# Kernel optimization log

Measured on AMD Instinct MI355X. Metric: run time of the kernel, lower is better.

Reference implementation:

```python
import jax, jax.numpy as jnp
import numpy as np

N = 65536   # total nodes
E = 1048576 # total edges (avg degree 16)
B = 512     # graphs in batch
H = 4       # gat1 heads
C = 64      # per-head channels / GNN_HIDDEN


def segment_softmax(logits, seg, num_segments):
    # numerically stable softmax over segments (PyG softmax semantics, eps=1e-16)
    m = jax.ops.segment_max(logits, seg, num_segments=num_segments)
    m = jnp.where(jnp.isfinite(m), m, 0.0)
    e = jnp.exp(logits - m[seg])
    s = jax.ops.segment_sum(e, seg, num_segments=num_segments)
    return e / (s[seg] + 1e-16)


def gat_conv(x, edge_index, edge_attr, W, att_src, att_dst, We, att_edge, bias, heads, out_ch, concat):
    # PyG GATConv with edge_dim, add_self_loops=False
    n = x.shape[0]
    h = (x @ W).reshape(n, heads, out_ch)                 # (N,H,C)
    src, dst = edge_index[0], edge_index[1]
    a_s = jnp.sum(h * att_src, axis=-1)                   # (N,H)
    a_d = jnp.sum(h * att_dst, axis=-1)                   # (N,H)
    he = (edge_attr @ We).reshape(-1, heads, out_ch)      # (E,H,C)
    a_e = jnp.sum(he * att_edge, axis=-1)                 # (E,H)
    alpha = jax.nn.leaky_relu(a_s[src] + a_d[dst] + a_e, negative_slope=0.2)
    alpha = segment_softmax(alpha, dst, n)                # softmax over incoming edges per dst
    out = jax.ops.segment_sum(h[src] * alpha[..., None], dst, num_segments=n)  # (N,H,C)
    out = out.reshape(n, heads * out_ch) if concat else out.mean(axis=1)
    return out + bias


def setup_inputs() -> dict:
    key = jax.random.key(0)
    ks = jax.random.split(key, 24)
    s = 0.05
    d = {}
    d["global_feat"] = jax.random.normal(ks[0], (B, 512), jnp.float32)
    d["x"] = jax.random.normal(ks[1], (N, 13), jnp.float32)
    d["roi_feats"] = jax.random.normal(ks[2], (N, 256), jnp.float32)
    d["edge_index"] = jax.random.randint(ks[3], (2, E), 0, N)
    d["edge_attr"] = jax.random.normal(ks[4], (E, 5), jnp.float32)
    d["batch_vec"] = jnp.sort(jax.random.randint(ks[5], (N,), 0, B))
    # roi_proj / scene_proj
    d["roi_W"] = jax.random.normal(ks[6], (256, 64), jnp.float32) * s
    d["roi_b"] = jnp.zeros((64,), jnp.float32)
    d["scene_W"] = jax.random.normal(ks[7], (512, 128), jnp.float32) * s
    d["scene_b"] = jnp.zeros((128,), jnp.float32)
    d["g1_W"] = jax.random.normal(ks[8], (77, H * C), jnp.float32) * s
    d["g1_att_src"] = jax.random.normal(ks[9], (H, C), jnp.float32) * s
    d["g1_att_dst"] = jax.random.normal(ks[10], (H, C), jnp.float32) * s
    d["g1_We"] = jax.random.normal(ks[11], (5, H * C), jnp.float32) * s
    d["g1_att_edge"] = jax.random.normal(ks[12], (H, C), jnp.float32) * s
    d["g1_bias"] = jnp.zeros((H * C,), jnp.float32)
    # gat2: 256 -> 64, 1 head
    d["g2_W"] = jax.random.normal(ks[13], (H * C, C), jnp.float32) * s
    d["g2_att_src"] = jax.random.normal(ks[14], (1, C), jnp.float32) * s
    d["g2_att_dst"] = jax.random.normal(ks[15], (1, C), jnp.float32) * s
    d["g2_We"] = jax.random.normal(ks[16], (5, C), jnp.float32) * s
    d["g2_att_edge"] = jax.random.normal(ks[17], (1, C), jnp.float32) * s
    d["g2_bias"] = jnp.zeros((C,), jnp.float32)
    # attention pooling gate + classifier
    d["gate_W"] = jax.random.normal(ks[18], (C, 1), jnp.float32) * s
    d["gate_b"] = jnp.zeros((1,), jnp.float32)
    d["cls1_W"] = jax.random.normal(ks[19], (128 + C, 64), jnp.float32) * s
    d["cls1_b"] = jnp.zeros((64,), jnp.float32)
    d["cls2_W"] = jax.random.normal(ks[20], (64, 3), jnp.float32) * s
    d["cls2_b"] = jnp.zeros((3,), jnp.float32)
    return d


def reference(global_feat, x, roi_feats, edge_index, edge_attr, batch_vec,
              roi_W, roi_b, scene_W, scene_b,
              g1_W, g1_att_src, g1_att_dst, g1_We, g1_att_edge, g1_bias,
              g2_W, g2_att_src, g2_att_dst, g2_We, g2_att_edge, g2_bias,
              gate_W, gate_b, cls1_W, cls1_b, cls2_W, cls2_b):
    scene = global_feat @ scene_W + scene_b                       # (B,128)
    vis = jax.nn.relu(roi_feats @ roi_W + roi_b)                  # (N,64)
    h = jnp.concatenate([x, vis], axis=-1)                        # (N,77)
    h = jax.nn.relu(gat_conv(h, edge_index, edge_attr, g1_W, g1_att_src, g1_att_dst, g1_We, g1_att_edge, g1_bias, H, C, True))
    h = gat_conv(h, edge_index, edge_attr, g2_W, g2_att_src, g2_att_dst, g2_We, g2_att_edge, g2_bias, 1, C, False)  # (N,64)
    # GlobalAttention pooling
    gate = segment_softmax((h @ gate_W + gate_b)[:, 0], batch_vec, B)
    rel = jax.ops.segment_sum(gate[:, None] * h, batch_vec, num_segments=B)  # (B,64)
    comb = jnp.concatenate([scene, rel], axis=-1)                 # (B,192)
    hid = jax.nn.relu(comb @ cls1_W + cls1_b)                     # dropout off (eval)
    return hid @ cls2_W + cls2_b                                  # (B,3)
```

## Files before the change

kernel.cpp:

```cpp
#include <hip/hip_runtime.h>

#define N_NODES 65536
#define N_EDGES 1048576
#define NB      512

typedef unsigned short u16;
typedef unsigned int   u32;
typedef unsigned long long u64;

__device__ __forceinline__ float bf2f(u16 u) { return __uint_as_float(((u32)u) << 16); }
__device__ __forceinline__ float lo16(u32 u) { return __uint_as_float(u << 16); }
__device__ __forceinline__ float hi16(u32 u) { return __uint_as_float(u & 0xffff0000u); }
__device__ __forceinline__ u16 f2bf(float f) {
    u32 u = __float_as_uint(f);
    u32 r = (u + 0x7fffu + ((u >> 16) & 1u)) >> 16;
    return (u16)r;
}
__device__ __forceinline__ float wsum(float v) {
    for (int o = 32; o; o >>= 1) v += __shfl_xor(v, o, 64);
    return v;
}
__device__ __forceinline__ float wmax(float v) {
    for (int o = 32; o; o >>= 1) v = fmaxf(v, __shfl_xor(v, o, 64));
    return v;
}

__global__ void k_prep(const float* g1We, const float* g1ae, const float* g2We, const float* g2ae,
                       float* M1, float* M2) {
    int t = threadIdx.x;
    if (t < 20) {
        int j = t >> 2, h = t & 3;
        float s = 0.f;
        for (int c = 0; c < 64; c++) s += g1We[j * 256 + h * 64 + c] * g1ae[h * 64 + c];
        M1[t] = s;
    } else if (t < 25) {
        int j = t - 20;
        float s = 0.f;
        for (int c = 0; c < 64; c++) s += g2We[j * 64 + c] * g2ae[c];
        M2[j] = s;
    }
}

__global__ __launch_bounds__(256) void k_scene(const float* __restrict__ gf, const float* __restrict__ W,
                                               const float* __restrict__ bias, float* __restrict__ scene) {
    int idx = blockIdx.x * 256 + threadIdx.x;
    int b = idx >> 7, j = idx & 127;
    float acc = 0.f;
    for (int k = 0; k < 512; k++) acc += gf[b * 512 + k] * W[k * 128 + j];
    scene[idx] = acc + bias[j];
}

__global__ __launch_bounds__(256) void k_hist(const int* ei, int* cnt) {
    int e = blockIdx.x * 256 + threadIdx.x;
    atomicAdd(&cnt[ei[N_EDGES + e]], 1);
}

__global__ __launch_bounds__(256) void k_scan_blk(const int* __restrict__ cnt, int* __restrict__ pre,
                                                  int* __restrict__ bsum) {
    __shared__ int sd[256];
    int t = threadIdx.x, b = blockIdx.x;
    int base = b * 1024 + t * 4;
    int4 c = *(const int4*)(cnt + base);
    int s = c.x + c.y + c.z + c.w;
    sd[t] = s;
    __syncthreads();
    for (int off = 1; off < 256; off <<= 1) {
        int v = (t >= off) ? sd[t - off] : 0;
        __syncthreads();
        sd[t] += v;
        __syncthreads();
    }
    int excl = sd[t] - s;
    int4 p;
    p.x = excl;
    p.y = excl + c.x;
    p.z = excl + c.x + c.y;
    p.w = excl + c.x + c.y + c.z;
    *(int4*)(pre + base) = p;
    if (t == 255) bsum[b] = sd[255];
}

__global__ __launch_bounds__(64) void k_scan_top(int* bsum) {
    int t = threadIdx.x;
    int v = bsum[t];
    int inc = v;
    for (int off = 1; off < 64; off <<= 1) {
        int u = __shfl_up(inc, off, 64);
        if (t >= off) inc += u;
    }
    bsum[t] = inc - v;
}

__global__ __launch_bounds__(256) void k_scan_fix(const int* __restrict__ pre, const int* __restrict__ bsum,
                                                  int* __restrict__ row_ptr, int* __restrict__ coarse_cur) {
    int i = blockIdx.x * 256 + threadIdx.x;
    int v = pre[i] + bsum[i >> 10];
    row_ptr[i] = v;
    if ((i & 255) == 0) coarse_cur[i >> 8] = v;
    if (i == 0) row_ptr[N_NODES] = N_EDGES;
}

__global__ __launch_bounds__(256) void k_bucket(const int* __restrict__ ei, int* coarse_cur,
                                                u32* __restrict__ bpack, int* __restrict__ bsrc) {
    __shared__ u32 stageP[4096];
    __shared__ int stageS[4096];
    __shared__ int bcnt[256], bscan[256], boff[256], gbase[256];
    int t = threadIdx.x;
    int e0 = blockIdx.x * 4096;
    bcnt[t] = 0;
    __syncthreads();
    int dreg[16], sreg[16];
    for (int it = 0; it < 16; it++) {
        int e = e0 + it * 256 + t;
        int dd = ei[N_EDGES + e];
        dreg[it] = dd;
        sreg[it] = ei[e];
        atomicAdd(&bcnt[dd >> 8], 1);
    }
    __syncthreads();
    int v = bcnt[t];
    bscan[t] = v;
    __syncthreads();
    for (int off = 1; off < 256; off <<= 1) {
        int u = (t >= off) ? bscan[t - off] : 0;
        __syncthreads();
        bscan[t] += u;
        __syncthreads();
    }
    boff[t] = bscan[t] - v;
    gbase[t] = v ? atomicAdd(&coarse_cur[t], v) : 0;
    __syncthreads();
    for (int it = 0; it < 16; it++) {
        int e = e0 + it * 256 + t;
        int b = dreg[it] >> 8;
        int pos = atomicAdd(&boff[b], 1);
        stageP[pos] = ((u32)e << 12) | (u32)(dreg[it] & 255);
        stageS[pos] = sreg[it];
    }
    __syncthreads();
    for (int idx = t; idx < 4096; idx += 256) {
        int lo = 0, hi = 255;
        while (lo < hi) { int mid = (lo + hi) >> 1; if (bscan[mid] > idx) hi = mid; else lo = mid + 1; }
        int b = lo;
        int g = gbase[b] + (idx - (bscan[b] - bcnt[b]));
        bpack[g] = stageP[idx];
        bsrc[g] = stageS[idx];
    }
}

__global__ __launch_bounds__(256) void k_sortb(const u32* __restrict__ bpack, const int* __restrict__ bsrc,
                                               const int* __restrict__ row_ptr,
                                               int* __restrict__ eord, int* __restrict__ ssrc) {
    __shared__ int cur[256];
    int t = threadIdx.x, b = blockIdx.x;
    int nbase = b * 256;
    cur[t] = row_ptr[nbase + t];
    __syncthreads();
    int beg = row_ptr[nbase];
    int end = row_ptr[nbase + 256];
    for (int i = beg + t; i < end; i += 256) {
        u32 wd = bpack[i];
        int src = bsrc[i];
        int d8 = wd & 255;
        int pos = atomicAdd(&cur[d8], 1);
        eord[pos] = (int)(wd >> 12);
        ssrc[pos] = src;
    }
}

__global__ __launch_bounds__(256) void k_payload(const int* __restrict__ eord, const float* __restrict__ ea,
                                                 const float* __restrict__ M1, const float* __restrict__ M2,
                                                 float* __restrict__ a1es, float* __restrict__ a2es) {
    int pos = blockIdx.x * 256 + threadIdx.x;
    int e = eord[pos];
    float v[5];
    for (int j = 0; j < 5; j++) v[j] = ea[(size_t)e * 5 + j];
    float4 o;
    o.x = v[0]*M1[0]  + v[1]*M1[4]  + v[2]*M1[8]  + v[3]*M1[12] + v[4]*M1[16];
    o.y = v[0]*M1[1]  + v[1]*M1[5]  + v[2]*M1[9]  + v[3]*M1[13] + v[4]*M1[17];
    o.z = v[0]*M1[2]  + v[1]*M1[6]  + v[2]*M1[10] + v[3]*M1[14] + v[4]*M1[18];
    o.w = v[0]*M1[3]  + v[1]*M1[7]  + v[2]*M1[11] + v[3]*M1[15] + v[4]*M1[19];
    *(float4*)(a1es + (size_t)pos * 4) = o;
    a2es[pos] = v[0]*M2[0] + v[1]*M2[1] + v[2]*M2[2] + v[3]*M2[3] + v[4]*M2[4];
}

__global__ __launch_bounds__(256) void k_vis(const float* __restrict__ A, const float* __restrict__ W,
                                             const float* __restrict__ bias, float* __restrict__ out) {
    __shared__ float At[64][68];
    __shared__ float Wl[64][68];
    int t = threadIdx.x;
    int n0 = blockIdx.x * 64;
    int cg = t & 15, rg = t >> 4;
    int sr = t >> 2, scs = (t & 3) * 16;
    float acc[4][4];
    for (int i = 0; i < 4; i++) for (int j = 0; j < 4; j++) acc[i][j] = 0.f;
    for (int kc = 0; kc < 4; kc++) {
        __syncthreads();
        const float* ap = A + (size_t)(n0 + sr) * 256 + kc * 64 + scs;
        float4 q0 = *(const float4*)ap, q1 = *(const float4*)(ap + 4);
        float4 q2 = *(const float4*)(ap + 8), q3 = *(const float4*)(ap + 12);
        At[scs + 0][sr] = q0.x;  At[scs + 1][sr] = q0.y;  At[scs + 2][sr] = q0.z;  At[scs + 3][sr] = q0.w;
        At[scs + 4][sr] = q1.x;  At[scs + 5][sr] = q1.y;  At[scs + 6][sr] = q1.z;  At[scs + 7][sr] = q1.w;
        At[scs + 8][sr] = q2.x;  At[scs + 9][sr] = q2.y;  At[scs + 10][sr] = q2.z; At[scs + 11][sr] = q2.w;
        At[scs + 12][sr] = q3.x; At[scs + 13][sr] = q3.y; At[scs + 14][sr] = q3.z; At[scs + 15][sr] = q3.w;
        const float* wp = W + (size_t)(kc * 64 + sr) * 64 + scs;
        *(float4*)&Wl[sr][scs + 0]  = *(const float4*)wp;
        *(float4*)&Wl[sr][scs + 4]  = *(const float4*)(wp + 4);
        *(float4*)&Wl[sr][scs + 8]  = *(const float4*)(wp + 8);
        *(float4*)&Wl[sr][scs + 12] = *(const float4*)(wp + 12);
        __syncthreads();
        for (int k = 0; k < 64; k++) {
            float4 a4 = *(const float4*)&At[k][rg * 4];
            float4 w4 = *(const float4*)&Wl[k][cg * 4];
            acc[0][0] += a4.x * w4.x; acc[0][1] += a4.x * w4.y; acc[0][2] += a4.x * w4.z; acc[0][3] += a4.x * w4.w;
            acc[1][0] += a4.y * w4.x; acc[1][1] += a4.y * w4.y; acc[1][2] += a4.y * w4.z; acc[1][3] += a4.y * w4.w;
            acc[2][0] += a4.z * w4.x; acc[2][1] += a4.z * w4.y; acc[2][2] += a4.z * w4.z; acc[2][3] += a4.z * w4.w;
            acc[3][0] += a4.w * w4.x; acc[3][1] += a4.w * w4.y; acc[3][2] += a4.w * w4.z; acc[3][3] += a4.w * w4.w;
        }
    }
    float4 bb = *(const float4*)(bias + cg * 4);
    for (int i = 0; i < 4; i++) {
        float4 o;
        o.x = fmaxf(acc[i][0] + bb.x, 0.f);
        o.y = fmaxf(acc[i][1] + bb.y, 0.f);
        o.z = fmaxf(acc[i][2] + bb.z, 0.f);
        o.w = fmaxf(acc[i][3] + bb.w, 0.f);
        *(float4*)(out + (size_t)(n0 + rg * 4 + i) * 64 + cg * 4) = o;
    }
}

__global__ __launch_bounds__(256) void k_h2(const u16* __restrict__ A, const float* __restrict__ W,
                                            u16* __restrict__ out) {
    __shared__ float At[64][68];
    __shared__ float Wl[64][68];
    int t = threadIdx.x;
    int n0 = blockIdx.x * 64;
    int cg = t & 15, rg = t >> 4;
    int sr = t >> 2, scs = (t & 3) * 16;
    float acc[4][4];
    for (int i = 0; i < 4; i++) for (int j = 0; j < 4; j++) acc[i][j] = 0.f;
    for (int kc = 0; kc < 4; kc++) {
        __syncthreads();
        const u16* ap = A + (size_t)(n0 + sr) * 256 + kc * 64 + scs;
        uint4 u0 = *(const uint4*)ap;
        uint4 u1 = *(const uint4*)(ap + 8);
        At[scs + 0][sr] = lo16(u0.x);  At[scs + 1][sr] = hi16(u0.x);
        At[scs + 2][sr] = lo16(u0.y);  At[scs + 3][sr] = hi16(u0.y);
        At[scs + 4][sr] = lo16(u0.z);  At[scs + 5][sr] = hi16(u0.z);
        At[scs + 6][sr] = lo16(u0.w);  At[scs + 7][sr] = hi16(u0.w);
        At[scs + 8][sr] = lo16(u1.x);  At[scs + 9][sr] = hi16(u1.x);
        At[scs + 10][sr] = lo16(u1.y); At[scs + 11][sr] = hi16(u1.y);
        At[scs + 12][sr] = lo16(u1.z); At[scs + 13][sr] = hi16(u1.z);
        At[scs + 14][sr] = lo16(u1.w); At[scs + 15][sr] = hi16(u1.w);
        const float* wp = W + (size_t)(kc * 64 + sr) * 64 + scs;
        *(float4*)&Wl[sr][scs + 0]  = *(const float4*)wp;
        *(float4*)&Wl[sr][scs + 4]  = *(const float4*)(wp + 4);
        *(float4*)&Wl[sr][scs + 8]  = *(const float4*)(wp + 8);
        *(float4*)&Wl[sr][scs + 12] = *(const float4*)(wp + 12);
        __syncthreads();
        for (int k = 0; k < 64; k++) {
            float4 a4 = *(const float4*)&At[k][rg * 4];
            float4 w4 = *(const float4*)&Wl[k][cg * 4];
            acc[0][0] += a4.x * w4.x; acc[0][1] += a4.x * w4.y; acc[0][2] += a4.x * w4.z; acc[0][3] += a4.x * w4.w;
            acc[1][0] += a4.y * w4.x; acc[1][1] += a4.y * w4.y; acc[1][2] += a4.y * w4.z; acc[1][3] += a4.y * w4.w;
            acc[2][0] += a4.z * w4.x; acc[2][1] += a4.z * w4.y; acc[2][2] += a4.z * w4.z; acc[2][3] += a4.z * w4.w;
            acc[3][0] += a4.w * w4.x; acc[3][1] += a4.w * w4.y; acc[3][2] += a4.w * w4.z; acc[3][3] += a4.w * w4.w;
        }
    }
    u32* outu = (u32*)out;
    for (int i = 0; i < 4; i++) {
        uint2 pk;
        pk.x = (u32)f2bf(acc[i][0]) | ((u32)f2bf(acc[i][1]) << 16);
        pk.y = (u32)f2bf(acc[i][2]) | ((u32)f2bf(acc[i][3]) << 16);
        *(uint2*)(outu + (size_t)(n0 + rg * 4 + i) * 32 + cg * 2) = pk;
    }
}

__global__ __launch_bounds__(256) void k_h1(const float* __restrict__ x, const float* __restrict__ vis,
                                            const float* __restrict__ g1W, u16* __restrict__ h1) {
    __shared__ float At[77][36];
    __shared__ float Wl[77][132];
    int t = threadIdx.x, ch = blockIdx.y;
    int n0 = blockIdx.x * 32;
    int cg = t & 31, rg = t >> 5;
    for (int idx = t; idx < 9856; idx += 256) {
        int k = idx >> 7, c = idx & 127;
        Wl[k][c] = g1W[(size_t)k * 256 + ch * 128 + c];
    }
    for (int idx = t; idx < 2464; idx += 256) {
        int r = idx / 77, k = idx - r * 77;
        At[k][r] = (k < 13) ? x[(size_t)(n0 + r) * 13 + k] : vis[(size_t)(n0 + r) * 64 + (k - 13)];
    }
    __syncthreads();
    float acc[4][4];
    for (int i = 0; i < 4; i++) for (int j = 0; j < 4; j++) acc[i][j] = 0.f;
    for (int k = 0; k < 77; k++) {
        float4 a4 = *(const float4*)&At[k][rg * 4];
        float4 w4 = *(const float4*)&Wl[k][cg * 4];
        acc[0][0] += a4.x * w4.x; acc[0][1] += a4.x * w4.y; acc[0][2] += a4.x * w4.z; acc[0][3] += a4.x * w4.w;
        acc[1][0] += a4.y * w4.x; acc[1][1] += a4.y * w4.y; acc[1][2] += a4.y * w4.z; acc[1][3] += a4.y * w4.w;
        acc[2][0] += a4.z * w4.x; acc[2][1] += a4.z * w4.y; acc[2][2] += a4.z * w4.z; acc[2][3] += a4.z * w4.w;
        acc[3][0] += a4.w * w4.x; acc[3][1] += a4.w * w4.y; acc[3][2] += a4.w * w4.z; acc[3][3] += a4.w * w4.w;
    }
    for (int i = 0; i < 4; i++) {
        uint2 pk;
        pk.x = (u32)f2bf(acc[i][0]) | ((u32)f2bf(acc[i][1]) << 16);
        pk.y = (u32)f2bf(acc[i][2]) | ((u32)f2bf(acc[i][3]) << 16);
        *(uint2*)(h1 + (size_t)(n0 + rg * 4 + i) * 256 + ch * 128 + cg * 4) = pk;
    }
}

__global__ __launch_bounds__(256) void k_a1(const u16* __restrict__ h1, const float* __restrict__ as_,
                                            const float* __restrict__ ad_, float* a1s, float* a1d) {
    int t = threadIdx.x;
    int w = t >> 6, L = t & 63;
    float4 as4 = *(const float4*)(as_ + 4 * L);
    float4 ad4 = *(const float4*)(ad_ + 4 * L);
    int base = (blockIdx.x * 4 + w) * 16;
    for (int j = 0; j < 16; j++) {
        int n = base + j;
        uint2 u = *((const uint2*)(h1 + (size_t)n * 256) + L);
        float v0 = lo16(u.x), v1 = hi16(u.x), v2 = lo16(u.y), v3 = hi16(u.y);
        float ps = v0 * as4.x + v1 * as4.y + v2 * as4.z + v3 * as4.w;
        float pd = v0 * ad4.x + v1 * ad4.y + v2 * ad4.z + v3 * ad4.w;
        for (int o = 1; o < 16; o <<= 1) { ps += __shfl_xor(ps, o, 64); pd += __shfl_xor(pd, o, 64); }
        if ((L & 15) == 0) {
            a1s[n * 4 + (L >> 4)] = ps;
            a1d[n * 4 + (L >> 4)] = pd;
        }
    }
}

__global__ __launch_bounds__(256) void k_a2(const u16* __restrict__ h2b, const float* __restrict__ as_,
                                            const float* __restrict__ ad_, float* a2s, float* a2d) {
    int t = threadIdx.x;
    int w = t >> 6, lane = t & 63;
    int n = blockIdx.x * 4 + w;
    float v = bf2f(h2b[(size_t)n * 64 + lane]);
    float ps = wsum(v * as_[lane]);
    float pd = wsum(v * ad_[lane]);
    if (lane == 0) { a2s[n] = ps; a2d[n] = pd; }
}

__global__ __launch_bounds__(256) void k_soft1(const int* __restrict__ row_ptr, const int* __restrict__ ssrc,
                                               const float* __restrict__ a1s, const float* __restrict__ a1d,
                                               const float* __restrict__ a1es, float* __restrict__ w1) {
    int t = threadIdx.x;
    int wv = t >> 6, L = t & 63;
    int n = blockIdx.x * 4 + wv;
    int h = L >> 4, j = L & 15;
    int beg = row_ptr[n], deg = row_ptr[n + 1] - beg;
    if (deg == 0) return;
    float adn = a1d[n * 4 + h];
    float m = -3.0e38f, s = 0.f;
    for (int i = j; i < deg; i += 16) {
        int pos = beg + i;
        float l = a1s[ssrc[pos] * 4 + h] + adn + a1es[(size_t)pos * 4 + h];
        l = (l > 0.f) ? l : 0.2f * l;
        if (l > m) { s = s * __expf(m - l) + 1.f; m = l; }
        else       { s += __expf(l - m); }
    }
    for (int o = 1; o < 16; o <<= 1) {
        float mo = __shfl_xor(m, o, 64), so = __shfl_xor(s, o, 64);
        float M = fmaxf(m, mo);
        s = s * __expf(m - M) + so * __expf(mo - M);
        m = M;
    }
    float inv = 1.f / (s + 1e-16f);
    for (int i = j; i < deg; i += 16) {
        int pos = beg + i;
        float l = a1s[ssrc[pos] * 4 + h] + adn + a1es[(size_t)pos * 4 + h];
        l = (l > 0.f) ? l : 0.2f * l;
        w1[(size_t)pos * 4 + h] = __expf(l - m) * inv;
    }
}

__global__ __launch_bounds__(256) void k_gath1(const int* __restrict__ row_ptr, const int* __restrict__ ssrc,
                                               const float* __restrict__ w1, const u16* __restrict__ h1,
                                               const float* __restrict__ bias, u16* __restrict__ out1) {
    int t = threadIdx.x;
    int wv = t >> 6, L = t & 63;
    int n = blockIdx.x * 4 + wv;
    int beg = row_ptr[n], deg = row_ptr[n + 1] - beg;
    int hd = L >> 4, j16 = L & 15;
    float a0 = 0.f, a1v = 0.f, a2v = 0.f, a3v = 0.f;
    int base = 0;
    for (; base + 16 <= deg; base += 16) {
        int idx = beg + base + j16;
        int src_r = ssrc[idx];
        float w_r = w1[(size_t)idx * 4 + hd];
        #pragma unroll
        for (int j = 0; j < 16; j++) {
            int src = __shfl(src_r, j, 64);
            float wgt = __shfl(w_r, hd * 16 + j, 64);
            uint2 ua = *((const uint2*)(h1 + (size_t)src * 256) + L);
            a0  += wgt * lo16(ua.x);
            a1v += wgt * hi16(ua.x);
            a2v += wgt * lo16(ua.y);
            a3v += wgt * hi16(ua.y);
        }
    }
    int cnt = deg - base;
    if (cnt > 0) {
        int idx = beg + base + j16;
        int src_r = 0; float w_r = 0.f;
        if (j16 < cnt) {
            src_r = ssrc[idx];
            w_r = w1[(size_t)idx * 4 + hd];
        }
        for (int j = 0; j < cnt; j++) {
            int src = __shfl(src_r, j, 64);
            float wgt = __shfl(w_r, hd * 16 + j, 64);
            uint2 ua = *((const uint2*)(h1 + (size_t)src * 256) + L);
            a0  += wgt * lo16(ua.x);
            a1v += wgt * hi16(ua.x);
            a2v += wgt * lo16(ua.y);
            a3v += wgt * hi16(ua.y);
        }
    }
    float4 bb = *(const float4*)(bias + 4 * L);
    uint2 pk;
    pk.x = (u32)f2bf(fmaxf(a0 + bb.x, 0.f)) | ((u32)f2bf(fmaxf(a1v + bb.y, 0.f)) << 16);
    pk.y = (u32)f2bf(fmaxf(a2v + bb.z, 0.f)) | ((u32)f2bf(fmaxf(a3v + bb.w, 0.f)) << 16);
    *((uint2*)(out1 + (size_t)n * 256) + L) = pk;
}

__global__ __launch_bounds__(256) void k_soft2(const int* __restrict__ row_ptr, const int* __restrict__ ssrc,
                                               const float* __restrict__ a2s, const float* __restrict__ a2d,
                                               const float* __restrict__ a2es, float* __restrict__ w2) {
    int t = threadIdx.x;
    int wv = t >> 6, L = t & 63;
    int g = L >> 4, j = L & 15;
    int n = blockIdx.x * 16 + wv * 4 + g;
    int beg = row_ptr[n], deg = row_ptr[n + 1] - beg;
    if (deg == 0) return;
    float adn = a2d[n];
    float m = -3.0e38f, s = 0.f;
    for (int i = j; i < deg; i += 16) {
        int pos = beg + i;
        float l = a2s[ssrc[pos]] + adn + a2es[pos];
        l = (l > 0.f) ? l : 0.2f * l;
        if (l > m) { s = s * __expf(m - l) + 1.f; m = l; }
        else       { s += __expf(l - m); }
    }
    for (int o = 1; o < 16; o <<= 1) {
        float mo = __shfl_xor(m, o, 64), so = __shfl_xor(s, o, 64);
        float M = fmaxf(m, mo);
        s = s * __expf(m - M) + so * __expf(mo - M);
        m = M;
    }
    float inv = 1.f / (s + 1e-16f);
    for (int i = j; i < deg; i += 16) {
        int pos = beg + i;
        float l = a2s[ssrc[pos]] + adn + a2es[pos];
        l = (l > 0.f) ? l : 0.2f * l;
        w2[pos] = __expf(l - m) * inv;
    }
}

__global__ __launch_bounds__(256) void k_gath2(const int* __restrict__ row_ptr, const int* __restrict__ ssrc,
                                               const float* __restrict__ w2, const u16* __restrict__ h2b,
                                               const float* __restrict__ bias, float* __restrict__ hfin) {
    int t = threadIdx.x;
    int wv = t >> 6, L = t & 63;
    int n = blockIdx.x * 4 + wv;
    int beg = row_ptr[n], deg = row_ptr[n + 1] - beg;
    float acc = 0.f;
    for (int base = 0; base < deg; base += 64) {
        int cnt = min(64, deg - base);
        int src_r = 0; float w_r = 0.f;
        if (L < cnt) {
            src_r = ssrc[beg + base + L];
            w_r = w2[beg + base + L];
        }
        int j = 0;
        for (; j + 4 <= cnt; j += 4) {
            int s0 = __shfl(src_r, j, 64),     s1 = __shfl(src_r, j + 1, 64);
            int s2 = __shfl(src_r, j + 2, 64), s3 = __shfl(src_r, j + 3, 64);
            float w0 = __shfl(w_r, j, 64),     w1v = __shfl(w_r, j + 1, 64);
            float w2v = __shfl(w_r, j + 2, 64), w3 = __shfl(w_r, j + 3, 64);
            float v0 = bf2f(h2b[(size_t)s0 * 64 + L]);
            float v1 = bf2f(h2b[(size_t)s1 * 64 + L]);
            float v2 = bf2f(h2b[(size_t)s2 * 64 + L]);
            float v3 = bf2f(h2b[(size_t)s3 * 64 + L]);
            acc += w0 * v0 + w1v * v1 + w2v * v2 + w3 * v3;
        }
        for (; j < cnt; j++) {
            int s0 = __shfl(src_r, j, 64);
            float w0 = __shfl(w_r, j, 64);
            acc += w0 * bf2f(h2b[(size_t)s0 * 64 + L]);
        }
    }
    hfin[(size_t)n * 64 + L] = acc + bias[L];
}

__global__ __launch_bounds__(64) void k_pool(const int* __restrict__ bvec, const float* __restrict__ hf,
                                             const float* gateW, const float* gateb,
                                             const float* __restrict__ scene,
                                             const float* c1W, const float* c1b,
                                             const float* c2W, const float* c2b,
                                             float* __restrict__ outp) {
    int b = blockIdx.x, lane = threadIdx.x;
    __shared__ float gwl[64], se[64], comb[192], hid[64];
    gwl[lane] = gateW[lane];
    __syncthreads();
    int s0, s1;
    { int lo = 0, hi = N_NODES; while (lo < hi) { int mid = (lo + hi) >> 1; if (bvec[mid] < b) lo = mid + 1; else hi = mid; } s0 = lo; }
    { int lo = 0, hi = N_NODES; while (lo < hi) { int mid = (lo + hi) >> 1; if (bvec[mid] < b + 1) lo = mid + 1; else hi = mid; } s1 = lo; }
    float gb = gateb[0];
    float m = -3.0e38f, ssum = 0.f, acc = 0.f;
    for (int cs = s0; cs < s1; cs += 64) {
        int cnt = min(64, s1 - cs);
        float l = -3.0e38f;
        if (lane < cnt) {
            int n = cs + lane;
            float d = 0.f;
            for (int i = 0; i < 64; i++) d += hf[(size_t)n * 64 + i] * gwl[i];
            l = d + gb;
        }
        float cm = wmax(l);
        float newm = fmaxf(m, cm);
        float rsc = __expf(m - newm);
        float e = (lane < cnt) ? __expf(l - newm) : 0.f;
        float es = wsum(e);
        ssum = ssum * rsc + es;
        se[lane] = e;
        __syncthreads();
        float a2 = 0.f;
        for (int i = 0; i < cnt; i++) a2 += se[i] * hf[(size_t)(cs + i) * 64 + lane];
        acc = acc * rsc + a2;
        __syncthreads();
        m = newm;
    }
    float rel = acc / (ssum + 1e-16f);
    comb[lane] = scene[b * 128 + lane];
    comb[64 + lane] = scene[b * 128 + 64 + lane];
    comb[128 + lane] = rel;
    __syncthreads();
    float hj = 0.f;
    for (int k = 0; k < 192; k++) hj += comb[k] * c1W[k * 64 + lane];
    hj += c1b[lane];
    hid[lane] = fmaxf(hj, 0.f);
    __syncthreads();
    if (lane < 3) {
        float o = 0.f;
        for (int k = 0; k < 64; k++) o += hid[k] * c2W[k * 3 + lane];
        o += c2b[lane];
        outp[b * 3 + lane] = o;
    }
}

extern "C" void kernel_launch(void* const* d_in, const int* in_sizes, int n_in,
                              void* d_out, int out_size, void* d_ws, size_t ws_size,
                              hipStream_t stream) {
    (void)in_sizes; (void)n_in; (void)out_size; (void)ws_size;
    const float* gf     = (const float*)d_in[0];
    const float* x      = (const float*)d_in[1];
    const float* roi    = (const float*)d_in[2];
    const int*   ei     = (const int*)d_in[3];
    const float* ea     = (const float*)d_in[4];
    const int*   bvec   = (const int*)d_in[5];
    const float* roiW   = (const float*)d_in[6];
    const float* roib   = (const float*)d_in[7];
    const float* sceneW = (const float*)d_in[8];
    const float* sceneb = (const float*)d_in[9];
    const float* g1W    = (const float*)d_in[10];
    const float* g1as   = (const float*)d_in[11];
    const float* g1ad   = (const float*)d_in[12];
    const float* g1We   = (const float*)d_in[13];
    const float* g1ae   = (const float*)d_in[14];
    const float* g1b    = (const float*)d_in[15];
    const float* g2W    = (const float*)d_in[16];
    const float* g2as   = (const float*)d_in[17];
    const float* g2ad   = (const float*)d_in[18];
    const float* g2We   = (const float*)d_in[19];
    const float* g2ae   = (const float*)d_in[20];
    const float* g2b    = (const float*)d_in[21];
    const float* gateW  = (const float*)d_in[22];
    const float* gateb  = (const float*)d_in[23];
    const float* c1W    = (const float*)d_in[24];
    const float* c1b    = (const float*)d_in[25];
    const float* c2W    = (const float*)d_in[26];
    const float* c2b    = (const float*)d_in[27];

    char* w = (char*)d_ws;
    size_t o = 0;
    auto nxt = [&](size_t bytes) -> char* {
        char* p = w + o;
        o += (bytes + 255) & ~(size_t)255;
        return p;
    };
    float* scene  = (float*)nxt((size_t)NB * 128 * 4);
    float* M1     = (float*)nxt(80);
    float* M2     = (float*)nxt(32);
    int* cnt      = (int*)nxt((size_t)N_NODES * 4);
    int* pre      = (int*)nxt((size_t)N_NODES * 4);
    int* bsum     = (int*)nxt(64 * 4);
    int* row_ptr  = (int*)nxt((size_t)(N_NODES + 1) * 4);
    int* coarse   = (int*)nxt(256 * 4);
    u32* bpack    = (u32*)nxt((size_t)N_EDGES * 4);
    int* bsrc     = (int*)nxt((size_t)N_EDGES * 4);
    int* eord     = (int*)nxt((size_t)N_EDGES * 4);
    int* ssrc     = (int*)nxt((size_t)N_EDGES * 4);
    float* a1es   = (float*)nxt((size_t)N_EDGES * 16);
    float* a2es   = (float*)nxt((size_t)N_EDGES * 4);
    float* visbuf = (float*)nxt((size_t)N_NODES * 64 * 4);
    u16* h1       = (u16*)nxt((size_t)N_NODES * 256 * 2);
    u16* out1     = (u16*)nxt((size_t)N_NODES * 256 * 2);
    float* w1buf  = (float*)nxt((size_t)N_EDGES * 16);
    float* hfin   = (float*)nxt((size_t)N_NODES * 64 * 4);
    float* a1s    = (float*)nxt((size_t)N_NODES * 16);
    float* a1d    = (float*)nxt((size_t)N_NODES * 16);
    float* a2s    = (float*)nxt((size_t)N_NODES * 4);
    float* a2d    = (float*)nxt((size_t)N_NODES * 4);

    float* vis = visbuf;
    float* w2  = visbuf;
    float* w1  = w1buf;
    u16*   h2b = (u16*)w1buf;

    hipMemsetAsync(cnt, 0, (size_t)N_NODES * 4, stream);
    k_prep<<<1, 32, 0, stream>>>(g1We, g1ae, g2We, g2ae, M1, M2);
    k_scene<<<(NB * 128) / 256, 256, 0, stream>>>(gf, sceneW, sceneb, scene);
    k_hist<<<N_EDGES / 256, 256, 0, stream>>>(ei, cnt);
    k_scan_blk<<<64, 256, 0, stream>>>(cnt, pre, bsum);
    k_scan_top<<<1, 64, 0, stream>>>(bsum);
    k_scan_fix<<<N_NODES / 256, 256, 0, stream>>>(pre, bsum, row_ptr, coarse);
    k_bucket<<<256, 256, 0, stream>>>(ei, coarse, bpack, bsrc);
    k_sortb<<<256, 256, 0, stream>>>(bpack, bsrc, row_ptr, eord, ssrc);
    k_payload<<<N_EDGES / 256, 256, 0, stream>>>(eord, ea, M1, M2, a1es, a2es);
    k_vis<<<N_NODES / 64, 256, 0, stream>>>(roi, roiW, roib, vis);
    k_h1<<<dim3(N_NODES / 32, 2), 256, 0, stream>>>(x, vis, g1W, h1);
    k_a1<<<N_NODES / 64, 256, 0, stream>>>(h1, g1as, g1ad, a1s, a1d);
    k_soft1<<<N_NODES / 4, 256, 0, stream>>>(row_ptr, ssrc, a1s, a1d, a1es, w1);
    k_gath1<<<N_NODES / 4, 256, 0, stream>>>(row_ptr, ssrc, w1, h1, g1b, out1);
    k_h2<<<N_NODES / 64, 256, 0, stream>>>(out1, g2W, h2b);
    k_a2<<<N_NODES / 4, 256, 0, stream>>>(h2b, g2as, g2ad, a2s, a2d);
    k_soft2<<<N_NODES / 16, 256, 0, stream>>>(row_ptr, ssrc, a2s, a2d, a2es, w2);
    k_gath2<<<N_NODES / 4, 256, 0, stream>>>(row_ptr, ssrc, w2, h2b, g2b, hfin);
    k_pool<<<NB, 64, 0, stream>>>(bvec, hfin, gateW, gateb, scene, c1W, c1b, c2W, c2b, (float*)d_out);
}
```

Before: 657.8 us.

## Split wavefront into two edge-halves with wider row loads in GAT gathers

Both gather kernels now split each 64-lane wavefront into two 32-lane halves that process different edges at once. Each lane loads wider vectors: 16 bytes per lane for the 4-head layer and 4 bytes for the 64-channel layer. Each half handles two edges per iteration, and the halves' partial sums are combined with a cross-half shuffle before the bias and store. The intent is more memory-level parallelism and fewer, wider random row loads per edge, replacing the shuffle-broadcast of indices with direct per-lane index loads. Costs include redundant index and weight loads across lanes, more accumulator registers, and a final reduction step.

Result: faster. 640.9 us (-2.6%).

```diff
diff --git a/kernel.cpp b/kernel.cpp
--- a/kernel.cpp
+++ b/kernel.cpp
@@ -382,47 +382,44 @@
     int wv = t >> 6, L = t & 63;
     int n = blockIdx.x * 4 + wv;
     int beg = row_ptr[n], deg = row_ptr[n + 1] - beg;
-    int hd = L >> 4, j16 = L & 15;
-    float a0 = 0.f, a1v = 0.f, a2v = 0.f, a3v = 0.f;
-    int base = 0;
-    for (; base + 16 <= deg; base += 16) {
-        int idx = beg + base + j16;
-        int src_r = ssrc[idx];
-        float w_r = w1[(size_t)idx * 4 + hd];
-        #pragma unroll
-        for (int j = 0; j < 16; j++) {
-            int src = __shfl(src_r, j, 64);
-            float wgt = __shfl(w_r, hd * 16 + j, 64);
-            uint2 ua = *((const uint2*)(h1 + (size_t)src * 256) + L);
-            a0  += wgt * lo16(ua.x);
-            a1v += wgt * hi16(ua.x);
-            a2v += wgt * lo16(ua.y);
-            a3v += wgt * hi16(ua.y);
-        }
-    }
-    int cnt = deg - base;
-    if (cnt > 0) {
-        int idx = beg + base + j16;
-        int src_r = 0; float w_r = 0.f;
-        if (j16 < cnt) {
-            src_r = ssrc[idx];
-            w_r = w1[(size_t)idx * 4 + hd];
-        }
-        for (int j = 0; j < cnt; j++) {
-            int src = __shfl(src_r, j, 64);
-            float wgt = __shfl(w_r, hd * 16 + j, 64);
-            uint2 ua = *((const uint2*)(h1 + (size_t)src * 256) + L);
-            a0  += wgt * lo16(ua.x);
-            a1v += wgt * hi16(ua.x);
-            a2v += wgt * lo16(ua.y);
-            a3v += wgt * hi16(ua.y);
-        }
-    }
-    float4 bb = *(const float4*)(bias + 4 * L);
-    uint2 pk;
-    pk.x = (u32)f2bf(fmaxf(a0 + bb.x, 0.f)) | ((u32)f2bf(fmaxf(a1v + bb.y, 0.f)) << 16);
-    pk.y = (u32)f2bf(fmaxf(a2v + bb.z, 0.f)) | ((u32)f2bf(fmaxf(a3v + bb.w, 0.f)) << 16);
-    *((uint2*)(out1 + (size_t)n * 256) + L) = pk;
+    int halfE = L >> 5;
+    int L32 = L & 31;
+    int hd = L32 >> 3;
+    float acc[8];
+    #pragma unroll
+    for (int j = 0; j < 8; j++) acc[j] = 0.f;
+    int last = beg + deg - 1;
+    for (int i = 0; i < deg; i += 4) {
+        int iA = i + halfE, iB = i + 2 + halfE;
+        int pA = beg + iA, pB = beg + iB;
+        bool vA = iA < deg, vB = iB < deg;
+        int cA = vA ? pA : last, cB = vB ? pB : last;
+        int sA = ssrc[cA], sB = ssrc[cB];
+        float wA = vA ? w1[(size_t)cA * 4 + hd] : 0.f;
+        float wB = vB ? w1[(size_t)cB * 4 + hd] : 0.f;
+        uint4 uA = *((const uint4*)(h1 + (size_t)sA * 256) + L32);
+        uint4 uB = *((const uint4*)(h1 + (size_t)sB * 256) + L32);
+        acc[0] += wA * lo16(uA.x) + wB * lo16(uB.x);
+        acc[1] += wA * hi16(uA.x) + wB * hi16(uB.x);
+        acc[2] += wA * lo16(uA.y) + wB * lo16(uB.y);
+        acc[3] += wA * hi16(uA.y) + wB * hi16(uB.y);
+        acc[4] += wA * lo16(uA.z) + wB * lo16(uB.z);
+        acc[5] += wA * hi16(uA.z) + wB * hi16(uB.z);
+        acc[6] += wA * lo16(uA.w) + wB * lo16(uB.w);
+        acc[7] += wA * hi16(uA.w) + wB * hi16(uB.w);
+    }
+    #pragma unroll
+    for (int j = 0; j < 8; j++) acc[j] += __shfl_xor(acc[j], 32, 64);
+    if (halfE == 0) {
+        float4 b0 = *(const float4*)(bias + 8 * L32);
+        float4 b1 = *(const float4*)(bias + 8 * L32 + 4);
+        uint4 pk;
+        pk.x = (u32)f2bf(fmaxf(acc[0] + b0.x, 0.f)) | ((u32)f2bf(fmaxf(acc[1] + b0.y, 0.f)) << 16);
+        pk.y = (u32)f2bf(fmaxf(acc[2] + b0.z, 0.f)) | ((u32)f2bf(fmaxf(acc[3] + b0.w, 0.f)) << 16);
+        pk.z = (u32)f2bf(fmaxf(acc[4] + b1.x, 0.f)) | ((u32)f2bf(fmaxf(acc[5] + b1.y, 0.f)) << 16);
+        pk.w = (u32)f2bf(fmaxf(acc[6] + b1.z, 0.f)) | ((u32)f2bf(fmaxf(acc[7] + b1.w, 0.f)) << 16);
+        *((uint4*)(out1 + (size_t)n * 256) + L32) = pk;
+    }
 }
 
 __global__ __launch_bounds__(256) void k_soft2(const int* __restrict__ row_ptr, const int* __restrict__ ssrc,
@@ -465,33 +462,32 @@
     int wv = t >> 6, L = t & 63;
     int n = blockIdx.x * 4 + wv;
     int beg = row_ptr[n], deg = row_ptr[n + 1] - beg;
-    float acc = 0.f;
-    for (int base = 0; base < deg; base += 64) {
-        int cnt = min(64, deg - base);
-        int src_r = 0; float w_r = 0.f;
-        if (L < cnt) {
-            src_r = ssrc[beg + base + L];
-            w_r = w2[beg + base + L];
-        }
-        int j = 0;
-        for (; j + 4 <= cnt; j += 4) {
-            int s0 = __shfl(src_r, j, 64),     s1 = __shfl(src_r, j + 1, 64);
-            int s2 = __shfl(src_r, j + 2, 64), s3 = __shfl(src_r, j + 3, 64);
-            float w0 = __shfl(w_r, j, 64),     w1v = __shfl(w_r, j + 1, 64);
-            float w2v = __shfl(w_r, j + 2, 64), w3 = __shfl(w_r, j + 3, 64);
-            float v0 = bf2f(h2b[(size_t)s0 * 64 + L]);
-            float v1 = bf2f(h2b[(size_t)s1 * 64 + L]);
-            float v2 = bf2f(h2b[(size_t)s2 * 64 + L]);
-            float v3 = bf2f(h2b[(size_t)s3 * 64 + L]);
-            acc += w0 * v0 + w1v * v1 + w2v * v2 + w3 * v3;
-        }
-        for (; j < cnt; j++) {
-            int s0 = __shfl(src_r, j, 64);
-            float w0 = __shfl(w_r, j, 64);
-            acc += w0 * bf2f(h2b[(size_t)s0 * 64 + L]);
-        }
-    }
-    hfin[(size_t)n * 64 + L] = acc + bias[L];
+    int halfE = L >> 5;
+    int L32 = L & 31;
+    float a0 = 0.f, a1v = 0.f;
+    int last = beg + deg - 1;
+    const u32* h2u = (const u32*)h2b;
+    for (int i = 0; i < deg; i += 4) {
+        int iA = i + halfE, iB = i + 2 + halfE;
+        int pA = beg + iA, pB = beg + iB;
+        bool vA = iA < deg, vB = iB < deg;
+        int cA = vA ? pA : last, cB = vB ? pB : last;
+        int sA = ssrc[cA], sB = ssrc[cB];
+        float wA = vA ? w2[cA] : 0.f;
+        float wB = vB ? w2[cB] : 0.f;
+        u32 uA = h2u[(size_t)sA * 32 + L32];
+        u32 uB = h2u[(size_t)sB * 32 + L32];
+        a0  += wA * lo16(uA) + wB * lo16(uB);
+        a1v += wA * hi16(uA) + wB * hi16(uB);
+    }
+    a0  += __shfl_xor(a0, 32, 64);
+    a1v += __shfl_xor(a1v, 32, 64);
+    if (halfE == 0) {
+        float2 o;
+        o.x = a0  + bias[2 * L32];
+        o.y = a1v + bias[2 * L32 + 1];
+        *(float2*)(hfin + (size_t)n * 64 + 2 * L32) = o;
+    }
 }
 
 __global__ __launch_bounds__(64) void k_pool(const int* __restrict__ bvec, const float* __restrict__ hf,
```
